# Kernel tuning notes

Measured on AMD Instinct MI355X. Metric: run time of the kernel, lower is better.

The kernel has to match this reference:

```python
import jax, jax.numpy as jnp
import numpy as np

DIM, H, HD = 512, 8, 64
N_BANK = 4096
EPS = 1e-5


def layernorm(x, g, b):
    m = jnp.mean(x, axis=-1, keepdims=True)
    v = jnp.mean(jnp.square(x - m), axis=-1, keepdims=True)
    return (x - m) * jax.lax.rsqrt(v + EPS) * g + b


def setup_inputs() -> dict:
    key = jax.random.key(0)
    ks = jax.random.split(key, 8)
    # xavier_uniform bound for square (512,512) linears
    bound = float(np.sqrt(6.0 / (DIM + DIM)))
    inp = {
        "x_q": jax.random.normal(ks[0], (32, 128, DIM), jnp.float32),
        "x_k": jax.random.normal(ks[1], (N_BANK, DIM), jnp.float32),
        "x_v": jax.random.normal(ks[2], (N_BANK, DIM), jnp.float32),
        "Wq": jax.random.uniform(ks[3], (DIM, DIM), jnp.float32, -bound, bound),
        "Wk": jax.random.uniform(ks[4], (DIM, DIM), jnp.float32, -bound, bound),
        "Wv": jax.random.uniform(ks[5], (DIM, DIM), jnp.float32, -bound, bound),
        "Wproj": jax.random.uniform(ks[6], (DIM, DIM), jnp.float32, -bound, bound),
        "qn_g": jnp.ones((HD,), jnp.float32),
        "qn_b": jnp.zeros((HD,), jnp.float32),
        "kn_g": jnp.ones((HD,), jnp.float32),
        "kn_b": jnp.zeros((HD,), jnp.float32),
        "n_g": jnp.ones((DIM,), jnp.float32),
        "n_b": jnp.zeros((DIM,), jnp.float32),
    }
    return inp


def reference(x_q, x_k, x_v, Wq, Wk, Wv, Wproj, qn_g, qn_b, kn_g, kn_b, n_g, n_b):
    B, S, D = x_q.shape
    N = x_k.shape[0]
    scale = HD ** (-0.5)
    # Linear layers (torch: y = x @ W.T)
    q = jnp.einsum('bsd,od->bso', x_q, Wq).reshape(B, S, H, HD).transpose(0, 2, 1, 3)  # (B,H,S,hd)
    k = jnp.einsum('nd,od->no', x_k, Wk).reshape(N, H, HD).transpose(1, 0, 2)          # (H,N,hd)
    v = jnp.einsum('nd,od->no', x_v, Wv).reshape(N, H, HD).transpose(1, 0, 2)          # (H,N,hd)
    # per-head qk layernorm
    q = layernorm(q, qn_g, qn_b) * scale
    k = layernorm(k, kn_g, kn_b)
    # cross-attention to shared bank (K/V have no batch dim)
    attn = jnp.einsum('bhsd,hnd->bhsn', q, k)          # (B,H,S,N)
    attn = jax.nn.softmax(attn, axis=-1)
    x = jnp.einsum('bhsn,hnd->bhsd', attn, v)          # (B,H,S,hd)
    x = x.transpose(0, 2, 1, 3).reshape(B, S, D)
    x = layernorm(x, n_g, n_b)
    x = jnp.einsum('bsd,od->bso', x, Wproj)
    return x
```

## Files before the change

kernel.cpp:

```cpp
#include <hip/hip_runtime.h>
#include <hip/hip_bf16.h>
#include <math.h>

#define DIM 512
#define NHEAD 8
#define HD 64
#define NBANK 4096
#define NQROWS 4096
#define EPS 1e-5f
#define QSCALE 0.18033688011f
#define PART_ELEMS (NQROWS * DIM)

typedef __attribute__((ext_vector_type(4))) float floatx4;
typedef __attribute__((ext_vector_type(8))) short short8;

#if defined(__has_builtin)
#if __has_builtin(__builtin_amdgcn_exp2f)
#define EXP2(x) __builtin_amdgcn_exp2f(x)
#endif
#endif
#ifndef EXP2
#define EXP2(x) exp2f(x)
#endif

__device__ __forceinline__ unsigned short f2bf(float f) {
    unsigned int u = __float_as_uint(f);
    u += 0x7fffu + ((u >> 16) & 1u);
    return (unsigned short)(u >> 16);
}
__device__ __forceinline__ float bf2f(unsigned short h) {
    return __uint_as_float(((unsigned int)h) << 16);
}
__device__ __forceinline__ unsigned int pk2(float a, float b) {
    union { __hip_bfloat162 h; unsigned int u; } cvt;
    cvt.h = __float22bfloat162_rn(make_float2(a, b));
    return cvt.u;
}
__device__ __forceinline__ void dma16(const void* gsrc, void* ldst) {
    __builtin_amdgcn_global_load_lds(
        (const __attribute__((address_space(1))) unsigned int*)gsrc,
        (__attribute__((address_space(3))) unsigned int*)ldst, 16, 0, 0);
}

__global__ __launch_bounds__(256) void cvt_kernel(
    const float* __restrict__ Wq, const float* __restrict__ Wk,
    const float* __restrict__ Wv, const float* __restrict__ Wp,
    const float* __restrict__ xq, const float* __restrict__ xk,
    const float* __restrict__ xv,
    unsigned short* __restrict__ Wb, unsigned short* __restrict__ Xb)
{
    const int y = blockIdx.y;
    const float* src;
    unsigned short* dst;
    if (y < 4) {
        if (blockIdx.x >= 128) return;
        src = (y == 0) ? Wq : (y == 1) ? Wk : (y == 2) ? Wv : Wp;
        dst = Wb + (size_t)y * DIM * DIM;
    } else {
        src = (y == 4) ? xq : (y == 5) ? xk : xv;
        dst = Xb + (size_t)(y - 4) * NQROWS * DIM;
    }
    const int i = (blockIdx.x * 256 + threadIdx.x) * 8;
    const int row = i >> 9, kpos = i & 511;
    const int kt = kpos >> 6, seg = (kpos >> 3) & 7;
    const float4 a0 = *(const float4*)(src + i);
    const float4 a1 = *(const float4*)(src + i + 4);
    union { short8 v; unsigned int u[4]; } t;
    t.u[0] = pk2(a0.x, a0.y); t.u[1] = pk2(a0.z, a0.w);
    t.u[2] = pk2(a1.x, a1.y); t.u[3] = pk2(a1.z, a1.w);
    *(short8*)(dst + (size_t)row * 512 + kt * 64 + ((seg ^ (row & 7)) << 3)) = t.v;
}

__global__ __launch_bounds__(256) void qkv_kernel(
    const unsigned short* __restrict__ Xb, const unsigned short* __restrict__ Wb,
    const float* __restrict__ qg, const float* __restrict__ qbeta,
    const float* __restrict__ kg, const float* __restrict__ kbeta,
    unsigned short* __restrict__ Qb, unsigned short* __restrict__ Kb,
    unsigned short* __restrict__ VTb)
{
    __shared__ short8 smem[3072];
    const int tid  = threadIdx.x;
    const int w    = tid >> 6, lane = tid & 63, m = lane & 15, q = lane >> 4;
    const int wr   = w & 1, wc = w >> 1;
    const int row0 = blockIdx.x * 64;
    const int mat  = blockIdx.y >> 2;
    const int col0 = (blockIdx.y & 3) * 128;
    const unsigned short* Xm = Xb + (size_t)mat * NQROWS * DIM;
    const unsigned short* Wm = Wb + (size_t)mat * DIM * DIM;

    const int it0 = tid, it1 = tid + 256;
    const unsigned short* asrc0 = Xm + (size_t)(row0 + (it0 >> 3)) * DIM + (it0 & 7) * 8;
    const unsigned short* asrc1 = Xm + (size_t)(row0 + (it1 >> 3)) * DIM + (it1 & 7) * 8;
    const unsigned short* bsrc[4];
    #pragma unroll
    for (int j = 0; j < 4; ++j) {
        const int item = j * 256 + tid;
        bsrc[j] = Wm + (size_t)(col0 + (item >> 3)) * DIM + (item & 7) * 8;
    }

    floatx4 acc[2][4];
    #pragma unroll
    for (int mt = 0; mt < 2; ++mt)
        #pragma unroll
        for (int nt = 0; nt < 4; ++nt) acc[mt][nt] = (floatx4){0.f, 0.f, 0.f, 0.f};

    {
        short8* as = smem; short8* bs = smem + 512;
        dma16(asrc0, as + w * 64);
        dma16(asrc1, as + 256 + w * 64);
        #pragma unroll
        for (int j = 0; j < 4; ++j)
            dma16(bsrc[j], bs + j * 256 + w * 64);
    }
    __syncthreads();

    for (int kt = 0; kt < 8; ++kt) {
        short8* as = smem + (kt & 1) * 1536;
        short8* bs = as + 512;
        if (kt < 7) {
            short8* asn = smem + ((kt + 1) & 1) * 1536;
            short8* bsn = asn + 512;
            const int o = (kt + 1) * 64;
            dma16(asrc0 + o, asn + w * 64);
            dma16(asrc1 + o, asn + 256 + w * 64);
            #pragma unroll
            for (int j = 0; j < 4; ++j)
                dma16(bsrc[j] + o, bsn + j * 256 + w * 64);
        }
        #pragma unroll
        for (int s = 0; s < 2; ++s) {
            short8 af[2], bfr[4];
            #pragma unroll
            for (int mt = 0; mt < 2; ++mt)
                af[mt] = as[(wr * 32 + mt * 16 + m) * 8 + ((s * 4 + q) ^ (m & 7))];
            #pragma unroll
            for (int nt = 0; nt < 4; ++nt)
                bfr[nt] = bs[(wc * 64 + nt * 16 + m) * 8 + ((s * 4 + q) ^ (m & 7))];
            #pragma unroll
            for (int mt = 0; mt < 2; ++mt)
                #pragma unroll
                for (int nt = 0; nt < 4; ++nt)
                    acc[mt][nt] = __builtin_amdgcn_mfma_f32_16x16x32_bf16(af[mt], bfr[nt], acc[mt][nt], 0, 0, 0);
        }
        __syncthreads();
    }

    if (mat < 2) {
        const float* g = (mat == 0) ? qg : kg;
        const float* be = (mat == 0) ? qbeta : kbeta;
        unsigned short* Y = (mat == 0) ? Qb : Kb;
        float gv[4], bv[4];
        #pragma unroll
        for (int nt = 0; nt < 4; ++nt) { gv[nt] = g[nt * 16 + m]; bv[nt] = be[nt * 16 + m]; }
        #pragma unroll
        for (int mt = 0; mt < 2; ++mt) {
            #pragma unroll
            for (int r = 0; r < 4; ++r) {
                float s = 0.f, sq = 0.f;
                #pragma unroll
                for (int nt = 0; nt < 4; ++nt) { const float v = acc[mt][nt][r]; s += v; sq += v * v; }
                s  += __shfl_xor(s, 1);  s  += __shfl_xor(s, 2);  s  += __shfl_xor(s, 4);  s  += __shfl_xor(s, 8);
                sq += __shfl_xor(sq, 1); sq += __shfl_xor(sq, 2); sq += __shfl_xor(sq, 4); sq += __shfl_xor(sq, 8);
                const float mean = s * (1.f / HD);
                const float var  = sq * (1.f / HD) - mean * mean;
                const float rr   = rsqrtf(var + EPS);
                const int grow = row0 + wr * 32 + mt * 16 + q * 4 + r;
                #pragma unroll
                for (int nt = 0; nt < 4; ++nt) {
                    float v = (acc[mt][nt][r] - mean) * rr * gv[nt] + bv[nt];
                    if (mat == 0) v *= QSCALE;
                    const int col = col0 + wc * 64 + nt * 16 + m;
                    int scol = col;
                    if (mat == 1) {
                        const int o = col & 63, sg2 = o >> 3;
                        scol = (col & ~63) | (((sg2 ^ (grow & 7)) << 3) | (o & 7));
                    }
                    Y[(size_t)grow * DIM + scol] = f2bf(v);
                }
            }
        }
    } else {
        unsigned short* vt = (unsigned short*)smem;
        __syncthreads();
        #pragma unroll
        for (int mt = 0; mt < 2; ++mt)
            #pragma unroll
            for (int nt = 0; nt < 4; ++nt) {
                const int c  = wc * 64 + nt * 16 + m;
                const int rw = wr * 32 + mt * 16 + q * 4;
                *(unsigned int*)(vt + c * 88 + rw)     = pk2(acc[mt][nt][0], acc[mt][nt][1]);
                *(unsigned int*)(vt + c * 88 + rw + 2) = pk2(acc[mt][nt][2], acc[mt][nt][3]);
            }
        __syncthreads();
        #pragma unroll
        for (int p = 0; p < 4; ++p) {
            const int idx = p * 256 + tid;
            const int c = idx >> 3, g = idx & 7;
            const int dglob = col0 + c, hh = dglob >> 6, dl = dglob & 63;
            const int pos = (g >> 2) * 32 + (g & 3) * 4;
            union { short8 v; ushort4 h4[2]; } tv;
            tv.h4[0] = *(const ushort4*)(vt + c * 88 + pos);
            tv.h4[1] = *(const ushort4*)(vt + c * 88 + pos + 16);
            *(short8*)(VTb + ((size_t)(hh * 64 + blockIdx.x) * 512
                              + dl * 8 + (g ^ (dl & 7))) * 8) = tv.v;
        }
    }
}

__global__ __launch_bounds__(256, 4) void attn_kernel(
    const unsigned short* __restrict__ Qb, const unsigned short* __restrict__ Kb,
    const unsigned short* __restrict__ VTb, unsigned short* __restrict__ AOp,
    float* __restrict__ sums)
{
    __shared__ short8 smem[2560];
    const int tid  = threadIdx.x;
    const int w    = tid >> 6;
    const int lane = tid & 63;
    const int m    = lane & 15;
    const int Qd   = lane >> 4;
    const int h    = blockIdx.x & 7;
    const int qgi  = blockIdx.x >> 3;
    const int row0 = qgi * 128;
    const int part = blockIdx.y;
    const int c0   = part * 16;

    const int it0 = tid, it1 = tid + 256;
    const unsigned short* ksrc0 = Kb + (size_t)(it0 >> 3) * DIM + h * HD + (it0 & 7) * 8;
    const unsigned short* ksrc1 = Kb + (size_t)(it1 >> 3) * DIM + h * HD + (it1 & 7) * 8;
    const unsigned short* vbase = VTb + (size_t)h * 64 * 512 * 8;

    short8 qf[2][2];
    #pragma unroll
    for (int mt = 0; mt < 2; ++mt)
        #pragma unroll
        for (int s = 0; s < 2; ++s)
            qf[mt][s] = *(const short8*)(Qb + (size_t)(row0 + w * 32 + mt * 16 + m) * DIM
                                         + h * HD + s * 32 + Qd * 8);

    floatx4 of[4][2];
    float sump[2] = {0.f, 0.f};
    #pragma unroll
    for (int t = 0; t < 4; ++t)
        #pragma unroll
        for (int mt = 0; mt < 2; ++mt) of[t][mt] = (floatx4){0.f, 0.f, 0.f, 0.f};
    const floatx4 fz = (floatx4){0.f, 0.f, 0.f, 0.f};

    {
        dma16(ksrc0 + (size_t)c0 * 64 * DIM, smem + w * 64);
        dma16(ksrc1 + (size_t)c0 * 64 * DIM, smem + 256 + w * 64);
        dma16(vbase + ((size_t)c0 * 512 + it0) * 8, smem + 1536 + w * 64);
        dma16(vbase + ((size_t)c0 * 512 + it1) * 8, smem + 1536 + 256 + w * 64);
        dma16(ksrc0 + ((size_t)c0 + 1) * 64 * DIM, smem + 512 + w * 64);
        dma16(ksrc1 + ((size_t)c0 + 1) * 64 * DIM, smem + 512 + 256 + w * 64);
    }

    #pragma unroll
    for (int c = 0; c < 16; ++c) {
        if (c < 15) asm volatile("s_waitcnt vmcnt(2)" ::: "memory");
        else        asm volatile("s_waitcnt vmcnt(0)" ::: "memory");
        __builtin_amdgcn_s_barrier();
        __builtin_amdgcn_sched_barrier(0);

        short8* ks  = smem + (c % 3) * 512;
        short8* vts = smem + 1536 + (c & 1) * 512;
        if (c < 15) {
            short8* vtsn = smem + 1536 + ((c + 1) & 1) * 512;
            const size_t nc = (size_t)(c0 + c + 1);
            dma16(vbase + (nc * 512 + it0) * 8, vtsn + w * 64);
            dma16(vbase + (nc * 512 + it1) * 8, vtsn + 256 + w * 64);
        }
        if (c < 14) {
            short8* ksn = smem + ((c + 2) % 3) * 512;
            const size_t nc2 = (size_t)(c0 + c + 2);
            dma16(ksrc0 + nc2 * 64 * DIM, ksn + w * 64);
            dma16(ksrc1 + nc2 * 64 * DIM, ksn + 256 + w * 64);
        }

        floatx4 st[4][2];
        #pragma unroll
        for (int t = 0; t < 4; ++t) {
            const short8 kf = ks[(t * 16 + m) * 8 + (Qd ^ (m & 7))];
            #pragma unroll
            for (int mt = 0; mt < 2; ++mt)
                st[t][mt] = __builtin_amdgcn_mfma_f32_16x16x32_bf16(kf, qf[mt][0], fz, 0, 0, 0);
        }
        #pragma unroll
        for (int t = 0; t < 4; ++t) {
            const short8 kf = ks[(t * 16 + m) * 8 + ((4 + Qd) ^ (m & 7))];
            #pragma unroll
            for (int mt = 0; mt < 2; ++mt)
                st[t][mt] = __builtin_amdgcn_mfma_f32_16x16x32_bf16(kf, qf[mt][1], st[t][mt], 0, 0, 0);
        }

        union { short8 v; unsigned int u[4]; } pf[2][2];
        #pragma unroll
        for (int mt = 0; mt < 2; ++mt)
            #pragma unroll
            for (int s2 = 0; s2 < 2; ++s2)
                #pragma unroll
                for (int u = 0; u < 4; ++u) {
                    const int t = s2 * 2 + (u >> 1), r = (u & 1) * 2;
                    const float e0 = EXP2(st[t][mt][r]);
                    const float e1 = EXP2(st[t][mt][r + 1]);
                    sump[mt] += e0;
                    sump[mt] += e1;
                    pf[mt][s2].u[u] = pk2(e0, e1);
                }

        #pragma unroll
        for (int s2 = 0; s2 < 2; ++s2)
            #pragma unroll
            for (int t2 = 0; t2 < 4; ++t2) {
                const short8 vf = vts[(t2 * 16 + m) * 8 + ((s2 * 4 + Qd) ^ (m & 7))];
                #pragma unroll
                for (int mt = 0; mt < 2; ++mt)
                    of[t2][mt] = __builtin_amdgcn_mfma_f32_16x16x32_bf16(vf, pf[mt][s2].v, of[t2][mt], 0, 0, 0);
            }
    }
    __syncthreads();

    #pragma unroll
    for (int mt = 0; mt < 2; ++mt) {
        float s = sump[mt];
        s += __shfl_xor(s, 16);
        s += __shfl_xor(s, 32);
        sump[mt] = s;
    }
    if (Qd == 0) {
        #pragma unroll
        for (int mt = 0; mt < 2; ++mt)
            sums[((size_t)part * NQROWS + row0 + w * 32 + mt * 16 + m) * NHEAD + h] = sump[mt];
    }

    unsigned int* ob = (unsigned int*)smem;
    #pragma unroll
    for (int t2 = 0; t2 < 4; ++t2)
        #pragma unroll
        for (int mt = 0; mt < 2; ++mt) {
            const int qq  = w * 32 + mt * 16 + m;
            const int blk = t2 * 2 + (Qd >> 1);
            const int sub = (Qd & 1) * 2;
            const int bs  = (blk ^ (qq & 7)) * 4;
            ob[qq * 32 + bs + sub]     = pk2(of[t2][mt][0], of[t2][mt][1]);
            ob[qq * 32 + bs + sub + 1] = pk2(of[t2][mt][2], of[t2][mt][3]);
        }
    __syncthreads();
    #pragma unroll
    for (int pp = 0; pp < 4; ++pp) {
        const int idx = tid + pp * 256;
        const int qq = idx >> 3, sg = idx & 7;
        *(short8*)(AOp + (size_t)part * PART_ELEMS + (size_t)(row0 + qq) * DIM + h * HD + sg * 8) =
            smem[qq * 8 + (sg ^ (qq & 7))];
    }
}

__global__ __launch_bounds__(256) void combine_kernel(
    const unsigned short* __restrict__ AOp, const float* __restrict__ sums,
    const float* __restrict__ g, const float* __restrict__ be,
    unsigned short* __restrict__ AO)
{
    __shared__ float rs[256], rq[256], sm[2], sr[2];
    const int tid  = threadIdx.x;
    const int half = tid >> 7;
    const int row  = blockIdx.x * 2 + half;
    const int t    = tid & 127;
    const int h    = t >> 4;

    float stot = 0.f;
    #pragma unroll
    for (int p = 0; p < 4; ++p)
        stot += sums[((size_t)p * NQROWS + row) * NHEAD + h];

    float o[4] = {0.f, 0.f, 0.f, 0.f};
    #pragma unroll
    for (int p = 0; p < 4; ++p) {
        const ushort4 u = *(const ushort4*)(AOp + (size_t)p * PART_ELEMS + (size_t)row * DIM + t * 4);
        o[0] += bf2f(u.x); o[1] += bf2f(u.y); o[2] += bf2f(u.z); o[3] += bf2f(u.w);
    }
    const float inv = 1.0f / stot;
    const float v0 = o[0] * inv, v1 = o[1] * inv, v2 = o[2] * inv, v3 = o[3] * inv;

    rs[tid] = v0 + v1 + v2 + v3;
    rq[tid] = v0 * v0 + v1 * v1 + v2 * v2 + v3 * v3;
    __syncthreads();
    #pragma unroll
    for (int off = 64; off > 0; off >>= 1) {
        if (t < off) { rs[tid] += rs[tid + off]; rq[tid] += rq[tid + off]; }
        __syncthreads();
    }
    if (t == 0) {
        const float mean = rs[tid] * (1.f / DIM);
        const float var  = rq[tid] * (1.f / DIM) - mean * mean;
        sm[half] = mean;
        sr[half] = rsqrtf(var + EPS);
    }
    __syncthreads();

    const float mean = sm[half], rstd = sr[half];
    const float4 g4 = *(const float4*)(g + t * 4);
    const float4 b4 = *(const float4*)(be + t * 4);
    uint2 packed;
    packed.x = pk2((v0 - mean) * rstd * g4.x + b4.x, (v1 - mean) * rstd * g4.y + b4.y);
    packed.y = pk2((v2 - mean) * rstd * g4.z + b4.z, (v3 - mean) * rstd * g4.w + b4.w);
    const int kt = t >> 4, seg = (t >> 1) & 7, jof = (t & 1) * 4;
    *(uint2*)(AO + (size_t)row * DIM + kt * 64 + ((seg ^ (row & 7)) << 3) + jof) = packed;
}

__global__ __launch_bounds__(256) void final_kernel(
    const unsigned short* __restrict__ AO, const unsigned short* __restrict__ Wpb,
    float* __restrict__ out)
{
    __shared__ short8 fs[3072];
    const int tid  = threadIdx.x;
    const int w    = tid >> 6, lane = tid & 63, m = lane & 15, q = lane >> 4;
    const int row0 = blockIdx.x * 64;
    const int col0 = blockIdx.y * 64;

    const int it0 = tid, it1 = tid + 256;
    const unsigned short* asrc0 = AO  + (size_t)(row0 + (it0 >> 3)) * DIM + (it0 & 7) * 8;
    const unsigned short* asrc1 = AO  + (size_t)(row0 + (it1 >> 3)) * DIM + (it1 & 7) * 8;
    const unsigned short* wsrc0 = Wpb + (size_t)(col0 + (it0 >> 3)) * DIM + (it0 & 7) * 8;
    const unsigned short* wsrc1 = Wpb + (size_t)(col0 + (it1 >> 3)) * DIM + (it1 & 7) * 8;

    floatx4 acc[4];
    #pragma unroll
    for (int mt = 0; mt < 4; ++mt) acc[mt] = (floatx4){0.f, 0.f, 0.f, 0.f};

    {
        dma16(asrc0, fs + w * 64);
        dma16(asrc1, fs + 256 + w * 64);
        dma16(wsrc0, fs + 512 + w * 64);
        dma16(wsrc1, fs + 768 + w * 64);
        dma16(asrc0 + 64, fs + 1024 + w * 64);
        dma16(asrc1 + 64, fs + 1024 + 256 + w * 64);
        dma16(wsrc0 + 64, fs + 1024 + 512 + w * 64);
        dma16(wsrc1 + 64, fs + 1024 + 768 + w * 64);
    }

    int cb = 0, nb = 2;
    for (int kt = 0; kt < 8; ++kt) {
        if (kt < 7) asm volatile("s_waitcnt vmcnt(4)" ::: "memory");
        else        asm volatile("s_waitcnt vmcnt(0)" ::: "memory");
        __builtin_amdgcn_s_barrier();
        __builtin_amdgcn_sched_barrier(0);

        short8* buf = fs + cb * 1024;
        if (kt < 6) {
            short8* bufn = fs + nb * 1024;
            const int o = (kt + 2) * 64;
            dma16(asrc0 + o, bufn + w * 64);
            dma16(asrc1 + o, bufn + 256 + w * 64);
            dma16(wsrc0 + o, bufn + 512 + w * 64);
            dma16(wsrc1 + o, bufn + 768 + w * 64);
        }
        #pragma unroll
        for (int s = 0; s < 2; ++s) {
            short8 af[4];
            #pragma unroll
            for (int mt = 0; mt < 4; ++mt)
                af[mt] = buf[(mt * 16 + m) * 8 + ((s * 4 + q) ^ (m & 7))];
            const short8 bfr = buf[512 + (w * 16 + m) * 8 + ((s * 4 + q) ^ (m & 7))];
            #pragma unroll
            for (int mt = 0; mt < 4; ++mt)
                acc[mt] = __builtin_amdgcn_mfma_f32_16x16x32_bf16(af[mt], bfr, acc[mt], 0, 0, 0);
        }
        cb = (cb == 2) ? 0 : cb + 1;
        nb = (nb == 2) ? 0 : nb + 1;
    }

    #pragma unroll
    for (int mt = 0; mt < 4; ++mt)
        #pragma unroll
        for (int r = 0; r < 4; ++r)
            out[(size_t)(row0 + mt * 16 + q * 4 + r) * DIM + col0 + w * 16 + m] = acc[mt][r];
}

extern "C" void kernel_launch(void* const* d_in, const int* in_sizes, int n_in,
                              void* d_out, int out_size, void* d_ws, size_t ws_size,
                              hipStream_t stream)
{
    const float* x_q = (const float*)d_in[0];
    const float* x_k = (const float*)d_in[1];
    const float* x_v = (const float*)d_in[2];
    const float* Wq  = (const float*)d_in[3];
    const float* Wk  = (const float*)d_in[4];
    const float* Wv  = (const float*)d_in[5];
    const float* Wp  = (const float*)d_in[6];
    const float* qg  = (const float*)d_in[7];
    const float* qb  = (const float*)d_in[8];
    const float* kg  = (const float*)d_in[9];
    const float* kb  = (const float*)d_in[10];
    const float* ng  = (const float*)d_in[11];
    const float* nb  = (const float*)d_in[12];
    float* out = (float*)d_out;

    unsigned short* Qb   = (unsigned short*)d_ws;
    unsigned short* Kb   = Qb  + (size_t)NQROWS * DIM;
    unsigned short* VTb  = Kb  + (size_t)NBANK * DIM;
    unsigned short* AOp  = VTb + (size_t)NBANK * DIM;
    float*          sums = (float*)(AOp + (size_t)4 * PART_ELEMS);
    unsigned short* Wb   = (unsigned short*)(sums + (size_t)4 * NQROWS * NHEAD);
    unsigned short* Xb   = AOp;
    unsigned short* AO   = Qb;

    cvt_kernel<<<dim3(1024, 7), 256, 0, stream>>>(Wq, Wk, Wv, Wp, x_q, x_k, x_v, Wb, Xb);
    qkv_kernel<<<dim3(64, 12), 256, 0, stream>>>(Xb, Wb, qg, qb, kg, kb, Qb, Kb, VTb);
    attn_kernel<<<dim3(256, 4), 256, 0, stream>>>(Qb, Kb, VTb, AOp, sums);
    combine_kernel<<<NQROWS / 2, 256, 0, stream>>>(AOp, sums, ng, nb, AO);
    final_kernel<<<dim3(64, 8), 256, 0, stream>>>(AO, Wb + (size_t)3 * DIM * DIM, out);
}
```

Baseline: 160.2 us.

## Use 512-thread attention blocks with software-pipelined QK and PV MFMAs

```diff
diff --git a/kernel.cpp b/kernel.cpp
--- a/kernel.cpp
+++ b/kernel.cpp
@@ -207,12 +207,12 @@
     }
 }
 
-__global__ __launch_bounds__(256, 4) void attn_kernel(
+__global__ __launch_bounds__(512, 4) void attn_kernel(
     const unsigned short* __restrict__ Qb, const unsigned short* __restrict__ Kb,
     const unsigned short* __restrict__ VTb, unsigned short* __restrict__ AOp,
     float* __restrict__ sums)
 {
-    __shared__ short8 smem[2560];
+    __shared__ short8 smem[4096];
     const int tid  = threadIdx.x;
     const int w    = tid >> 6;
     const int lane = tid & 63;
@@ -220,13 +220,11 @@
     const int Qd   = lane >> 4;
     const int h    = blockIdx.x & 7;
     const int qgi  = blockIdx.x >> 3;
-    const int row0 = qgi * 128;
+    const int row0 = qgi * 256;
     const int part = blockIdx.y;
     const int c0   = part * 16;
 
-    const int it0 = tid, it1 = tid + 256;
-    const unsigned short* ksrc0 = Kb + (size_t)(it0 >> 3) * DIM + h * HD + (it0 & 7) * 8;
-    const unsigned short* ksrc1 = Kb + (size_t)(it1 >> 3) * DIM + h * HD + (it1 & 7) * 8;
+    const unsigned short* ksrc  = Kb + (size_t)(tid >> 3) * DIM + h * HD + (tid & 7) * 8;
     const unsigned short* vbase = VTb + (size_t)h * 64 * 512 * 8;
 
     short8 qf[2][2];
@@ -244,78 +242,75 @@
         #pragma unroll
         for (int mt = 0; mt < 2; ++mt) of[t][mt] = (floatx4){0.f, 0.f, 0.f, 0.f};
     const floatx4 fz = (floatx4){0.f, 0.f, 0.f, 0.f};
-
-    {
-        dma16(ksrc0 + (size_t)c0 * 64 * DIM, smem + w * 64);
-        dma16(ksrc1 + (size_t)c0 * 64 * DIM, smem + 256 + w * 64);
-        dma16(vbase + ((size_t)c0 * 512 + it0) * 8, smem + 1536 + w * 64);
-        dma16(vbase + ((size_t)c0 * 512 + it1) * 8, smem + 1536 + 256 + w * 64);
-        dma16(ksrc0 + ((size_t)c0 + 1) * 64 * DIM, smem + 512 + w * 64);
-        dma16(ksrc1 + ((size_t)c0 + 1) * 64 * DIM, smem + 512 + 256 + w * 64);
-    }
-
-    #pragma unroll
-    for (int c = 0; c < 16; ++c) {
-        if (c < 15) asm volatile("s_waitcnt vmcnt(2)" ::: "memory");
-        else        asm volatile("s_waitcnt vmcnt(0)" ::: "memory");
+    union pfu { short8 v; unsigned int u[4]; };
+    pfu pf[2][2];
+
+    dma16(ksrc + (size_t)c0 * 64 * DIM,              smem + 0 * 512 + w * 64);
+    dma16(vbase + ((size_t)c0 * 512 + tid) * 8,      smem + 2048 + 0 * 512 + w * 64);
+    dma16(ksrc + ((size_t)c0 + 1) * 64 * DIM,        smem + 1 * 512 + w * 64);
+    dma16(vbase + (((size_t)c0 + 1) * 512 + tid) * 8, smem + 2048 + 1 * 512 + w * 64);
+
+    #pragma unroll
+    for (int c = 0; c <= 16; ++c) {
+        if (c <= 14)      asm volatile("s_waitcnt vmcnt(3)" ::: "memory");
+        else if (c == 15) asm volatile("s_waitcnt vmcnt(1)" ::: "memory");
+        else              asm volatile("s_waitcnt vmcnt(0)" ::: "memory");
         __builtin_amdgcn_s_barrier();
         __builtin_amdgcn_sched_barrier(0);
 
-        short8* ks  = smem + (c % 3) * 512;
-        short8* vts = smem + 1536 + (c & 1) * 512;
-        if (c < 15) {
-            short8* vtsn = smem + 1536 + ((c + 1) & 1) * 512;
-            const size_t nc = (size_t)(c0 + c + 1);
-            dma16(vbase + (nc * 512 + it0) * 8, vtsn + w * 64);
-            dma16(vbase + (nc * 512 + it1) * 8, vtsn + 256 + w * 64);
-        }
-        if (c < 14) {
-            short8* ksn = smem + ((c + 2) % 3) * 512;
-            const size_t nc2 = (size_t)(c0 + c + 2);
-            dma16(ksrc0 + nc2 * 64 * DIM, ksn + w * 64);
-            dma16(ksrc1 + nc2 * 64 * DIM, ksn + 256 + w * 64);
+        if (c <= 13) {
+            const size_t nc = (size_t)(c0 + c + 2);
+            dma16(ksrc + nc * 64 * DIM, smem + ((c + 2) & 3) * 512 + w * 64);
+            dma16(vbase + (nc * 512 + tid) * 8, smem + 2048 + ((c + 2) & 3) * 512 + w * 64);
         }
 
         floatx4 st[4][2];
-        #pragma unroll
-        for (int t = 0; t < 4; ++t) {
-            const short8 kf = ks[(t * 16 + m) * 8 + (Qd ^ (m & 7))];
+        __builtin_amdgcn_s_setprio(1);
+        if (c < 16) {
+            short8* ks = smem + (c & 3) * 512;
+            #pragma unroll
+            for (int t = 0; t < 4; ++t) {
+                const short8 kf = ks[(t * 16 + m) * 8 + (Qd ^ (m & 7))];
+                #pragma unroll
+                for (int mt = 0; mt < 2; ++mt)
+                    st[t][mt] = __builtin_amdgcn_mfma_f32_16x16x32_bf16(kf, qf[mt][0], fz, 0, 0, 0);
+            }
+            #pragma unroll
+            for (int t = 0; t < 4; ++t) {
+                const short8 kf = ks[(t * 16 + m) * 8 + ((4 + Qd) ^ (m & 7))];
+                #pragma unroll
+                for (int mt = 0; mt < 2; ++mt)
+                    st[t][mt] = __builtin_amdgcn_mfma_f32_16x16x32_bf16(kf, qf[mt][1], st[t][mt], 0, 0, 0);
+            }
+        }
+        if (c > 0) {
+            short8* vts = smem + 2048 + ((c - 1) & 3) * 512;
+            #pragma unroll
+            for (int s2 = 0; s2 < 2; ++s2)
+                #pragma unroll
+                for (int t2 = 0; t2 < 4; ++t2) {
+                    const short8 vf = vts[(t2 * 16 + m) * 8 + ((s2 * 4 + Qd) ^ (m & 7))];
+                    #pragma unroll
+                    for (int mt = 0; mt < 2; ++mt)
+                        of[t2][mt] = __builtin_amdgcn_mfma_f32_16x16x32_bf16(vf, pf[mt][s2].v, of[t2][mt], 0, 0, 0);
+                }
+        }
+        __builtin_amdgcn_s_setprio(0);
+        if (c < 16) {
             #pragma unroll
             for (int mt = 0; mt < 2; ++mt)
-                st[t][mt] = __builtin_amdgcn_mfma_f32_16x16x32_bf16(kf, qf[mt][0], fz, 0, 0, 0);
-        }
-        #pragma unroll
-        for (int t = 0; t < 4; ++t) {
-            const short8 kf = ks[(t * 16 + m) * 8 + ((4 + Qd) ^ (m & 7))];
-            #pragma unroll
-            for (int mt = 0; mt < 2; ++mt)
-                st[t][mt] = __builtin_amdgcn_mfma_f32_16x16x32_bf16(kf, qf[mt][1], st[t][mt], 0, 0, 0);
-        }
-
-        union { short8 v; unsigned int u[4]; } pf[2][2];
-        #pragma unroll
-        for (int mt = 0; mt < 2; ++mt)
-            #pragma unroll
-            for (int s2 = 0; s2 < 2; ++s2)
-                #pragma unroll
-                for (int u = 0; u < 4; ++u) {
-                    const int t = s2 * 2 + (u >> 1), r = (u & 1) * 2;
-                    const float e0 = EXP2(st[t][mt][r]);
-                    const float e1 = EXP2(st[t][mt][r + 1]);
-                    sump[mt] += e0;
-                    sump[mt] += e1;
-                    pf[mt][s2].u[u] = pk2(e0, e1);
-                }
-
-        #pragma unroll
-        for (int s2 = 0; s2 < 2; ++s2)
-            #pragma unroll
-            for (int t2 = 0; t2 < 4; ++t2) {
-                const short8 vf = vts[(t2 * 16 + m) * 8 + ((s2 * 4 + Qd) ^ (m & 7))];
-                #pragma unroll
-                for (int mt = 0; mt < 2; ++mt)
-                    of[t2][mt] = __builtin_amdgcn_mfma_f32_16x16x32_bf16(vf, pf[mt][s2].v, of[t2][mt], 0, 0, 0);
-            }
+                #pragma unroll
+                for (int s2 = 0; s2 < 2; ++s2)
+                    #pragma unroll
+                    for (int u = 0; u < 4; ++u) {
+                        const int t = s2 * 2 + (u >> 1), r = (u & 1) * 2;
+                        const float e0 = EXP2(st[t][mt][r]);
+                        const float e1 = EXP2(st[t][mt][r + 1]);
+                        sump[mt] += e0;
+                        sump[mt] += e1;
+                        pf[mt][s2].u[u] = pk2(e0, e1);
+                    }
+        }
     }
     __syncthreads();
 
@@ -347,7 +342,7 @@
     __syncthreads();
     #pragma unroll
     for (int pp = 0; pp < 4; ++pp) {
-        const int idx = tid + pp * 256;
+        const int idx = tid + pp * 512;
         const int qq = idx >> 3, sg = idx & 7;
         *(short8*)(AOp + (size_t)part * PART_ELEMS + (size_t)(row0 + qq) * DIM + h * HD + sg * 8) =
             smem[qq * 8 + (sg ^ (qq & 7))];
@@ -505,7 +500,7 @@
 
     cvt_kernel<<<dim3(1024, 7), 256, 0, stream>>>(Wq, Wk, Wv, Wp, x_q, x_k, x_v, Wb, Xb);
     qkv_kernel<<<dim3(64, 12), 256, 0, stream>>>(Xb, Wb, qg, qb, kg, kb, Qb, Kb, VTb);
-    attn_kernel<<<dim3(256, 4), 256, 0, stream>>>(Qb, Kb, VTb, AOp, sums);
+    attn_kernel<<<dim3(128, 4), 512, 0, stream>>>(Qb, Kb, VTb, AOp, sums);
     combine_kernel<<<NQROWS / 2, 256, 0, stream>>>(AOp, sums, ng, nb, AO);
     final_kernel<<<dim3(64, 8), 256, 0, stream>>>(AO, Wb + (size_t)3 * DIM * DIM, out);
 }
```

After: 156.6 us. 1.02x faster.
